# Kernel optimization log

Measured on AMD Instinct MI355X. Metric: run time of the kernel, lower is better.

Reference implementation:

```python
import jax, jax.numpy as jnp
import numpy as np

NUM_HEADS = 4
HIDDEN = 256
HEAD_DIM = HIDDEN // NUM_HEADS
N_NODES = 8192
N_EDGES = 262144
NEG = -1e9


def setup_inputs() -> dict:
    key = jax.random.key(0)
    ks = jax.random.split(key, 10)
    s = 1.0 / np.sqrt(HIDDEN)
    inp = {
        "node_features": jax.random.normal(ks[0], (N_NODES, HIDDEN), dtype=jnp.float32),
        "Wq": jax.random.uniform(ks[1], (HIDDEN, HIDDEN), jnp.float32, -s, s),
        "bq": jnp.zeros((HIDDEN,), jnp.float32),
        "Wk": jax.random.uniform(ks[2], (HIDDEN, HIDDEN), jnp.float32, -s, s),
        "bk": jnp.zeros((HIDDEN,), jnp.float32),
        "Wv": jax.random.uniform(ks[3], (HIDDEN, HIDDEN), jnp.float32, -s, s),
        "bv": jnp.zeros((HIDDEN,), jnp.float32),
        "Wo": jax.random.uniform(ks[4], (HIDDEN, HIDDEN), jnp.float32, -s, s),
        "bo": jnp.zeros((HIDDEN,), jnp.float32),
        "edge_index": jax.random.randint(ks[5], (2, N_EDGES), 0, N_NODES, dtype=jnp.int64),
    }
    return inp


def reference(node_features, Wq, bq, Wk, bk, Wv, bv, Wo, bo, edge_index):
    N = node_features.shape[0]
    # QKV projections -> [H, N, d]
    q = (node_features @ Wq + bq).reshape(N, NUM_HEADS, HEAD_DIM).transpose(1, 0, 2)
    k = (node_features @ Wk + bk).reshape(N, NUM_HEADS, HEAD_DIM).transpose(1, 0, 2)
    v = (node_features @ Wv + bv).reshape(N, NUM_HEADS, HEAD_DIM).transpose(1, 0, 2)
    # dense scores [H, N, N]
    scores = jnp.einsum('hnd,hmd->hnm', q, k) / jnp.sqrt(jnp.float32(HEAD_DIM))
    mask = jnp.full((N, N), NEG, dtype=jnp.float32).at[edge_index[0], edge_index[1]].set(0.0)
    scores = scores + mask[None, :, :]
    weights = jax.nn.softmax(scores, axis=-1)  # dropout is identity in eval
    context = jnp.einsum('hnm,hmd->hnd', weights, v)
    context = context.transpose(1, 0, 2).reshape(N, HIDDEN)
    return context @ Wo + bo
```

## Files before the change

kernel.cpp:

```cpp
#include <hip/hip_runtime.h>
#include <hip/hip_fp16.h>
#include <stdint.h>

#define NN 8192
#define HID 256
#define NH 4
#define HD 64
#define NE 262144
#define WPR (NN / 32)
#define CAP 128
#define NQKV 768
#define G1B 384

typedef __attribute__((ext_vector_type(8))) short s16x8;
typedef __attribute__((ext_vector_type(4))) float f32x4;
typedef _Float16 f16x2 __attribute__((ext_vector_type(2)));

__device__ __forceinline__ float fdot2(f16x2 a, f16x2 b, float c) {
#if __has_builtin(__builtin_amdgcn_fdot2)
    return __builtin_amdgcn_fdot2(a, b, c, false);
#else
    return c + (float)a.x * (float)b.x + (float)a.y * (float)b.y;
#endif
}

__device__ __forceinline__ void gload_lds16(const unsigned short* g, unsigned short* l) {
    __builtin_amdgcn_global_load_lds(
        (const __attribute__((address_space(1))) unsigned int*)g,
        (__attribute__((address_space(3))) unsigned int*)l, 16, 0, 0);
}

__global__ __launch_bounds__(256) void zero_kernel(uint4* __restrict__ p)
{
    p[blockIdx.x * 256 + threadIdx.x] = make_uint4(0, 0, 0, 0);
}

__global__ __launch_bounds__(256) void prep_kernel(
    const float* __restrict__ X,
    const float* __restrict__ Wq, const float* __restrict__ Wk,
    const float* __restrict__ Wv, const float* __restrict__ Wo,
    const float* __restrict__ bq, const float* __restrict__ bk,
    const float* __restrict__ bv, const int* __restrict__ ei,
    uint32_t* __restrict__ bitmap, unsigned short* __restrict__ Xh,
    unsigned short* __restrict__ W2Tq, unsigned short* __restrict__ W2To,
    float* __restrict__ biasq)
{
    const int b = blockIdx.x, tid = threadIdx.x;
    if (b < 1024) {
        int e = b * 256 + tid;
        int r = ei[e];
        int c = ei[NE + e];
        atomicOr(&bitmap[(size_t)r * WPR + (c >> 5)], 1u << (c & 31));
    } else if (b < 3072) {
        int i4 = ((b - 1024) * 256 + tid) * 4;
        float4 x = *(const float4*)(X + i4);
        __half2 h0 = __floats2half2_rn(x.x, x.y);
        __half2 h1 = __floats2half2_rn(x.z, x.w);
        uint2 w;
        w.x = *(unsigned*)&h0;
        w.y = *(unsigned*)&h1;
        *(uint2*)(Xh + i4) = w;
    } else {
        int lin = (b - 3072) * 256 + tid;
        int n = lin >> 8, k = lin & 255;
        const float* W; int ns; unsigned short* dst;
        if (n < NQKV) {
            W  = (n < 256) ? Wq : (n < 512) ? Wk : Wv;
            ns = n & 255;
            dst = W2Tq + (size_t)n * HID + k;
            if (k == 0) {
                const float* bsrc = (n < 256) ? bq : (n < 512) ? bk : bv;
                biasq[n] = bsrc[ns];
            }
        } else {
            W = Wo; ns = n - NQKV;
            dst = W2To + (size_t)ns * HID + k;
        }
        __half h = __float2half(W[(size_t)k * HID + ns]);
        *dst = *(unsigned short*)&h;
    }
}

template<int BN, bool HALF_OUT>
__device__ __forceinline__ void gemm_body(
    const unsigned short* __restrict__ A, const unsigned short* __restrict__ BT,
    const float* __restrict__ bias, void* __restrict__ Cv, int N,
    int m0, int n0, unsigned short* Alds, unsigned short* Blds)
{
    constexpr int NFR = BN / 32;
    const int tid  = threadIdx.x;
    const int lane = tid & 63, wave = tid >> 6;
    const int wm = wave >> 1, wn = wave & 1;

    const int r0 = tid >> 2, cc0 = tid & 3;
    const int r1 = (tid + 256) >> 2, cc1 = (tid + 256) & 3;

    f32x4 acc[4][NFR];
    #pragma unroll
    for (int i = 0; i < 4; ++i)
        #pragma unroll
        for (int j = 0; j < NFR; ++j)
            acc[i][j] = (f32x4){0.f, 0.f, 0.f, 0.f};

    for (int step = 0; step < 8; ++step) {
        const int kk = step * 32;
        __syncthreads();
        gload_lds16(A + (size_t)(m0 + r0) * HID + kk + cc0 * 8, &Alds[tid * 8]);
        gload_lds16(A + (size_t)(m0 + r1) * HID + kk + cc1 * 8, &Alds[(tid + 256) * 8]);
        gload_lds16(BT + (size_t)(n0 + r0) * HID + kk + cc0 * 8, &Blds[tid * 8]);
        if constexpr (BN == 128)
            gload_lds16(BT + (size_t)(n0 + r1) * HID + kk + cc1 * 8, &Blds[(tid + 256) * 8]);
        __syncthreads();

        s16x8 af[4], bfr[NFR];
        #pragma unroll
        for (int i = 0; i < 4; ++i)
            af[i] = *(const s16x8*)&Alds[(wm * 64 + i * 16 + (lane & 15)) * 32 + (lane >> 4) * 8];
        #pragma unroll
        for (int j = 0; j < NFR; ++j)
            bfr[j] = *(const s16x8*)&Blds[(wn * (BN / 2) + j * 16 + (lane & 15)) * 32 + (lane >> 4) * 8];
        #pragma unroll
        for (int i = 0; i < 4; ++i)
            #pragma unroll
            for (int j = 0; j < NFR; ++j)
                acc[i][j] = __builtin_amdgcn_mfma_f32_16x16x32_f16(af[i], bfr[j], acc[i][j], 0, 0, 0);
    }

    #pragma unroll
    for (int i = 0; i < 4; ++i) {
        #pragma unroll
        for (int j = 0; j < NFR; ++j) {
            int gcol = n0 + wn * (BN / 2) + j * 16 + (lane & 15);
            float bb = bias[gcol];
            #pragma unroll
            for (int r = 0; r < 4; ++r) {
                int grow = m0 + wm * 64 + i * 16 + (lane >> 4) * 4 + r;
                float v = acc[i][j][r] + bb;
                if constexpr (HALF_OUT)
                    ((__half*)Cv)[(size_t)grow * N + gcol] = __float2half(v);
                else
                    ((float*)Cv)[(size_t)grow * N + gcol] = v;
            }
        }
    }
}

__global__ __launch_bounds__(256) void gemm_csr_kernel(
    const unsigned short* __restrict__ Xh, const unsigned short* __restrict__ W2Tq,
    const float* __restrict__ biasq, __half* __restrict__ QKV,
    const uint32_t* __restrict__ bitmap, int* __restrict__ nbr, int* __restrict__ cnt)
{
    __shared__ __align__(16) unsigned short Alds[128 * 32];
    __shared__ __align__(16) unsigned short Blds[128 * 32];

    if (blockIdx.x < G1B) {
        constexpr int q8 = G1B >> 3;
        const int orig = blockIdx.x;
        const int id = (orig & 7) * q8 + (orig >> 3);
        gemm_body<128, true>(Xh, W2Tq, biasq, QKV, NQKV,
                             (id & 63) * 128, (id >> 6) * 128, Alds, Blds);
        return;
    }
    const int row = (blockIdx.x - G1B) * 4 + (threadIdx.x >> 6);
    const int lane = threadIdx.x & 63;
    const uint32_t* rp = bitmap + (size_t)row * WPR + lane * 4;
    uint32_t w0 = rp[0], w1 = rp[1], w2 = rp[2], w3 = rp[3];
    int pc = __popc(w0) + __popc(w1) + __popc(w2) + __popc(w3);
    int scan = pc;
    #pragma unroll
    for (int off = 1; off < 64; off <<= 1) {
        int t = __shfl_up(scan, off);
        if (lane >= off) scan += t;
    }
    int idx = scan - pc;
    int* dst = nbr + (size_t)row * CAP;
    const int base = lane * 128;
    uint32_t ws4[4] = {w0, w1, w2, w3};
    #pragma unroll
    for (int i = 0; i < 4; ++i) {
        uint32_t w = ws4[i];
        int cb = base + i * 32;
        while (w) {
            int b = __ffs(w) - 1;
            if (idx < CAP) dst[idx] = cb + b;
            ++idx;
            w &= w - 1;
        }
    }
    if (lane == 63) cnt[row] = min(scan, CAP);
}

template<int BN, bool HALF_OUT>
__global__ __launch_bounds__(256) void gemm_kernel(
    const unsigned short* __restrict__ A, const unsigned short* __restrict__ BT,
    const float* __restrict__ bias, void* __restrict__ Cv, int N)
{
    __shared__ __align__(16) unsigned short Alds[128 * 32];
    __shared__ __align__(16) unsigned short Blds[BN * 32];
    const int nwg = gridDim.x, orig = blockIdx.x, q8 = nwg >> 3;
    const int id = (orig & 7) * q8 + (orig >> 3);
    gemm_body<BN, HALF_OUT>(A, BT, bias, Cv, N,
                            (id & 63) * 128, (id >> 6) * BN, Alds, Blds);
}

__global__ __launch_bounds__(256) void attn_kernel(
    const __half* __restrict__ QKV, const int* __restrict__ nbr,
    const int* __restrict__ cntg, __half* __restrict__ ctx)
{
    const int row  = blockIdx.x * 4 + (threadIdx.x >> 6);
    const int lane = threadIdx.x & 63;
    const int cnt  = cntg[row];

    uint2 qraw = ((const uint2*)(QKV + (size_t)row * NQKV))[lane];
    union { uint2 u2; f16x2 h[2]; } uq; uq.u2 = qraw;
    const f16x2 q2a = uq.h[0], q2b = uq.h[1];

    float m = -INFINITY, l = 0.f;
    float a0 = 0.f, a1 = 0.f, a2 = 0.f, a3 = 0.f;

    for (int j0 = 0; j0 < cnt; j0 += 64) {
        int mynb = (j0 + lane < cnt) ? nbr[(size_t)row * CAP + j0 + lane] : 0;
        const int nb = min(64, cnt - j0);
        for (int b = 0; b < nb; b += 8) {
            int idx[8];
            #pragma unroll
            for (int u = 0; u < 8; ++u) idx[u] = __shfl(mynb, b + u);
            uint2 kv[8], vv[8];
            #pragma unroll
            for (int u = 0; u < 8; ++u) {
                const __half* base = QKV + (size_t)idx[u] * NQKV;
                kv[u] = ((const uint2*)(base + 256))[lane];
                vv[u] = ((const uint2*)(base + 512))[lane];
            }
            float s[8];
            #pragma unroll
            for (int u = 0; u < 8; ++u) {
                union { uint2 u2; f16x2 h[2]; } uk; uk.u2 = kv[u];
                float p = fdot2(q2a, uk.h[0], 0.f);
                p = fdot2(q2b, uk.h[1], p);
                #pragma unroll
                for (int off = 1; off < 16; off <<= 1) p += __shfl_xor(p, off);
                s[u] = (b + u < nb) ? p * 0.125f : -INFINITY;
            }
            float bm = s[0];
            #pragma unroll
            for (int u = 1; u < 8; ++u) bm = fmaxf(bm, s[u]);
            float mn = fmaxf(m, bm);
            float sc = expf(m - mn);
            a0 *= sc; a1 *= sc; a2 *= sc; a3 *= sc; l *= sc;
            #pragma unroll
            for (int u = 0; u < 8; ++u) {
                float w = expf(s[u] - mn);
                l += w;
                union { uint2 u2; __half2 h[2]; } uv; uv.u2 = vv[u];
                float2 f0 = __half22float2(uv.h[0]);
                float2 f1 = __half22float2(uv.h[1]);
                a0 = fmaf(w, f0.x, a0); a1 = fmaf(w, f0.y, a1);
                a2 = fmaf(w, f1.x, a2); a3 = fmaf(w, f1.y, a3);
            }
            m = mn;
        }
    }

    uint2 outw = make_uint2(0u, 0u);
    if (cnt > 0) {
        float rl = 1.f / l;
        __half2 o0 = __floats2half2_rn(a0 * rl, a1 * rl);
        __half2 o1 = __floats2half2_rn(a2 * rl, a3 * rl);
        outw.x = *(unsigned*)&o0;
        outw.y = *(unsigned*)&o1;
    }
    ((uint2*)(ctx + (size_t)row * HID))[lane] = outw;
}

extern "C" void kernel_launch(void* const* d_in, const int* in_sizes, int n_in,
                              void* d_out, int out_size, void* d_ws, size_t ws_size,
                              hipStream_t stream)
{
    const float* X  = (const float*)d_in[0];
    const float* Wq = (const float*)d_in[1];
    const float* bq = (const float*)d_in[2];
    const float* Wk = (const float*)d_in[3];
    const float* bk = (const float*)d_in[4];
    const float* Wv = (const float*)d_in[5];
    const float* bv = (const float*)d_in[6];
    const float* Wo = (const float*)d_in[7];
    const float* bo = (const float*)d_in[8];
    const int*   ei = (const int*)d_in[9];
    float* out = (float*)d_out;

    char* ws = (char*)d_ws;
    uint32_t*       bitmap = (uint32_t*)ws;
    __half*         QKV    = (__half*)(ws + 8388608);
    unsigned short* Xh     = (unsigned short*)(ws + 20971520);
    __half*         ctx    = (__half*)Xh;
    unsigned short* W2Tq   = (unsigned short*)(ws + 25165824);
    unsigned short* W2To   = (unsigned short*)(ws + 25559040);
    float*          biasq  = (float*)(ws + 25690112);
    int*            nbrL   = (int*)(ws + 25693184);
    int*            cntL   = (int*)(ws + 29887488);

    zero_kernel<<<2048, 256, 0, stream>>>((uint4*)bitmap);
    prep_kernel<<<4096, 256, 0, stream>>>(
        X, Wq, Wk, Wv, Wo, bq, bk, bv, ei, bitmap, Xh, W2Tq, W2To, biasq);
    gemm_csr_kernel<<<G1B + 2048, 256, 0, stream>>>(
        Xh, W2Tq, biasq, QKV, bitmap, nbrL, cntL);
    attn_kernel<<<NN / 4, 256, 0, stream>>>(QKV, nbrL, cntL, ctx);
    gemm_kernel<64, false><<<256, 256, 0, stream>>>(
        (const unsigned short*)ctx, W2To, bo, out, HID);
}
```

Measured before the change: 75.76 us.

## Fuse output projection GEMM into sparse attention kernel via LDS context tile

The attention kernel now processes 16 rows per 1024-thread block, stages the fp16 context rows in LDS, and then each wave computes a 16x16 slice of the output projection with MFMA against Wo read directly from global memory. This removes the separate output GEMM launch and the global write and read of the context buffer. In exchange, blocks are larger and synchronise after attention, so waves with fewer neighbours idle at the barrier. Wo fragments are also reloaded from global/L2 by every block instead of being shared through LDS tiles.

```diff
diff --git a/kernel.cpp b/kernel.cpp
--- a/kernel.cpp
+++ b/kernel.cpp
@@ -11,6 +11,7 @@
 #define CAP 128
 #define NQKV 768
 #define G1B 384
+#define CTXP 264
 
 typedef __attribute__((ext_vector_type(8))) short s16x8;
 typedef __attribute__((ext_vector_type(4))) float f32x4;
@@ -81,13 +82,11 @@
     }
 }
 
-template<int BN, bool HALF_OUT>
-__device__ __forceinline__ void gemm_body(
+__device__ __forceinline__ void gemm_body128(
     const unsigned short* __restrict__ A, const unsigned short* __restrict__ BT,
-    const float* __restrict__ bias, void* __restrict__ Cv, int N,
+    const float* __restrict__ bias, __half* __restrict__ Cv, int N,
     int m0, int n0, unsigned short* Alds, unsigned short* Blds)
 {
-    constexpr int NFR = BN / 32;
     const int tid  = threadIdx.x;
     const int lane = tid & 63, wave = tid >> 6;
     const int wm = wave >> 1, wn = wave & 1;
@@ -95,11 +94,11 @@
     const int r0 = tid >> 2, cc0 = tid & 3;
     const int r1 = (tid + 256) >> 2, cc1 = (tid + 256) & 3;
 
-    f32x4 acc[4][NFR];
+    f32x4 acc[4][4];
     #pragma unroll
     for (int i = 0; i < 4; ++i)
         #pragma unroll
-        for (int j = 0; j < NFR; ++j)
+        for (int j = 0; j < 4; ++j)
             acc[i][j] = (f32x4){0.f, 0.f, 0.f, 0.f};
 
     for (int step = 0; step < 8; ++step) {
@@ -108,38 +107,33 @@
         gload_lds16(A + (size_t)(m0 + r0) * HID + kk + cc0 * 8, &Alds[tid * 8]);
         gload_lds16(A + (size_t)(m0 + r1) * HID + kk + cc1 * 8, &Alds[(tid + 256) * 8]);
         gload_lds16(BT + (size_t)(n0 + r0) * HID + kk + cc0 * 8, &Blds[tid * 8]);
-        if constexpr (BN == 128)
-            gload_lds16(BT + (size_t)(n0 + r1) * HID + kk + cc1 * 8, &Blds[(tid + 256) * 8]);
+        gload_lds16(BT + (size_t)(n0 + r1) * HID + kk + cc1 * 8, &Blds[(tid + 256) * 8]);
         __syncthreads();
 
-        s16x8 af[4], bfr[NFR];
+        s16x8 af[4], bfr[4];
         #pragma unroll
         for (int i = 0; i < 4; ++i)
             af[i] = *(const s16x8*)&Alds[(wm * 64 + i * 16 + (lane & 15)) * 32 + (lane >> 4) * 8];
         #pragma unroll
-        for (int j = 0; j < NFR; ++j)
-            bfr[j] = *(const s16x8*)&Blds[(wn * (BN / 2) + j * 16 + (lane & 15)) * 32 + (lane >> 4) * 8];
+        for (int j = 0; j < 4; ++j)
+            bfr[j] = *(const s16x8*)&Blds[(wn * 64 + j * 16 + (lane & 15)) * 32 + (lane >> 4) * 8];
         #pragma unroll
         for (int i = 0; i < 4; ++i)
             #pragma unroll
-            for (int j = 0; j < NFR; ++j)
+            for (int j = 0; j < 4; ++j)
                 acc[i][j] = __builtin_amdgcn_mfma_f32_16x16x32_f16(af[i], bfr[j], acc[i][j], 0, 0, 0);
     }
 
     #pragma unroll
     for (int i = 0; i < 4; ++i) {
         #pragma unroll
-        for (int j = 0; j < NFR; ++j) {
-            int gcol = n0 + wn * (BN / 2) + j * 16 + (lane & 15);
+        for (int j = 0; j < 4; ++j) {
+            int gcol = n0 + wn * 64 + j * 16 + (lane & 15);
             float bb = bias[gcol];
             #pragma unroll
             for (int r = 0; r < 4; ++r) {
                 int grow = m0 + wm * 64 + i * 16 + (lane >> 4) * 4 + r;
-                float v = acc[i][j][r] + bb;
-                if constexpr (HALF_OUT)
-                    ((__half*)Cv)[(size_t)grow * N + gcol] = __float2half(v);
-                else
-                    ((float*)Cv)[(size_t)grow * N + gcol] = v;
+                Cv[(size_t)grow * N + gcol] = __float2half(acc[i][j][r] + bb);
             }
         }
     }
@@ -157,8 +151,8 @@
         constexpr int q8 = G1B >> 3;
         const int orig = blockIdx.x;
         const int id = (orig & 7) * q8 + (orig >> 3);
-        gemm_body<128, true>(Xh, W2Tq, biasq, QKV, NQKV,
-                             (id & 63) * 128, (id >> 6) * 128, Alds, Blds);
+        gemm_body128(Xh, W2Tq, biasq, QKV, NQKV,
+                     (id & 63) * 128, (id >> 6) * 128, Alds, Blds);
         return;
     }
     const int row = (blockIdx.x - G1B) * 4 + (threadIdx.x >> 6);
@@ -190,26 +184,18 @@
     if (lane == 63) cnt[row] = min(scan, CAP);
 }
 
-template<int BN, bool HALF_OUT>
-__global__ __launch_bounds__(256) void gemm_kernel(
-    const unsigned short* __restrict__ A, const unsigned short* __restrict__ BT,
-    const float* __restrict__ bias, void* __restrict__ Cv, int N)
-{
-    __shared__ __align__(16) unsigned short Alds[128 * 32];
-    __shared__ __align__(16) unsigned short Blds[BN * 32];
-    const int nwg = gridDim.x, orig = blockIdx.x, q8 = nwg >> 3;
-    const int id = (orig & 7) * q8 + (orig >> 3);
-    gemm_body<BN, HALF_OUT>(A, BT, bias, Cv, N,
-                            (id & 63) * 128, (id >> 6) * BN, Alds, Blds);
-}
-
-__global__ __launch_bounds__(256) void attn_kernel(
+__global__ __launch_bounds__(1024, 8) void attn_out_kernel(
     const __half* __restrict__ QKV, const int* __restrict__ nbr,
-    const int* __restrict__ cntg, __half* __restrict__ ctx)
-{
-    const int row  = blockIdx.x * 4 + (threadIdx.x >> 6);
+    const int* __restrict__ cntg, const unsigned short* __restrict__ W2To,
+    const float* __restrict__ bo, float* __restrict__ out)
+{
+    const int wv   = threadIdx.x >> 6;
     const int lane = threadIdx.x & 63;
+    const int rb   = blockIdx.x * 16;
+    const int row  = rb + wv;
     const int cnt  = cntg[row];
+
+    __shared__ __align__(16) unsigned short ctxlds[16][CTXP];
 
     uint2 qraw = ((const uint2*)(QKV + (size_t)row * NQKV))[lane];
     union { uint2 u2; f16x2 h[2]; } uq; uq.u2 = qraw;
@@ -262,15 +248,33 @@
         }
     }
 
-    uint2 outw = make_uint2(0u, 0u);
-    if (cnt > 0) {
-        float rl = 1.f / l;
+    {
+        float rl = (cnt > 0) ? (1.f / l) : 0.f;
         __half2 o0 = __floats2half2_rn(a0 * rl, a1 * rl);
         __half2 o1 = __floats2half2_rn(a2 * rl, a3 * rl);
-        outw.x = *(unsigned*)&o0;
-        outw.y = *(unsigned*)&o1;
-    }
-    ((uint2*)(ctx + (size_t)row * HID))[lane] = outw;
+        uint2 w;
+        w.x = *(unsigned*)&o0;
+        w.y = *(unsigned*)&o1;
+        *(uint2*)&ctxlds[wv][lane * 4] = w;
+    }
+    __syncthreads();
+
+    f32x4 acc = (f32x4){0.f, 0.f, 0.f, 0.f};
+    const unsigned short* bt = W2To + (size_t)(wv * 16 + (lane & 15)) * HID + (lane >> 4) * 8;
+    const unsigned short* al = &ctxlds[lane & 15][(lane >> 4) * 8];
+    #pragma unroll
+    for (int step = 0; step < 8; ++step) {
+        s16x8 af = *(const s16x8*)(al + step * 32);
+        s16x8 bf = *(const s16x8*)(bt + step * 32);
+        acc = __builtin_amdgcn_mfma_f32_16x16x32_f16(af, bf, acc, 0, 0, 0);
+    }
+    const int gcol = wv * 16 + (lane & 15);
+    const float bb = bo[gcol];
+    #pragma unroll
+    for (int r = 0; r < 4; ++r) {
+        int grow = rb + (lane >> 4) * 4 + r;
+        out[(size_t)grow * HID + gcol] = acc[r] + bb;
+    }
 }
 
 extern "C" void kernel_launch(void* const* d_in, const int* in_sizes, int n_in,
@@ -293,7 +297,6 @@
     uint32_t*       bitmap = (uint32_t*)ws;
     __half*         QKV    = (__half*)(ws + 8388608);
     unsigned short* Xh     = (unsigned short*)(ws + 20971520);
-    __half*         ctx    = (__half*)Xh;
     unsigned short* W2Tq   = (unsigned short*)(ws + 25165824);
     unsigned short* W2To   = (unsigned short*)(ws + 25559040);
     float*          biasq  = (float*)(ws + 25690112);
@@ -305,7 +308,6 @@
         X, Wq, Wk, Wv, Wo, bq, bk, bv, ei, bitmap, Xh, W2Tq, W2To, biasq);
     gemm_csr_kernel<<<G1B + 2048, 256, 0, stream>>>(
         Xh, W2Tq, biasq, QKV, bitmap, nbrL, cntL);
-    attn_kernel<<<NN / 4, 256, 0, stream>>>(QKV, nbrL, cntL, ctx);
-    gemm_kernel<64, false><<<256, 256, 0, stream>>>(
-        (const unsigned short*)ctx, W2To, bo, out, HID);
-}
+    attn_out_kernel<<<NN / 16, 1024, 0, stream>>>(
+        QKV, nbrL, cntL, W2To, bo, out);
+}
```

After: 78.25 us. 3.3% more time.

## Load K and V together as 16-byte vectors split across half-wavefronts

Applied to the files above, without the earlier changes.

Each wavefront lane now issues one 16-byte load over the contiguous K|V region of a neighbour row: lanes 0-31 hold K, lanes 32-63 hold V, 8 halves each. This replaces the two 8-byte loads per neighbour. The dot-product reduction becomes a 3-step butterfly within 8 lanes plus a cross-half exchange, and only the V half accumulates and writes output. It also adds a launch-bounds occupancy hint of 8 blocks. The aim is fewer memory instructions, at the cost of doubled accumulator registers and half the lanes doing redundant work in each phase.

```diff
diff --git a/kernel.cpp b/kernel.cpp
--- a/kernel.cpp
+++ b/kernel.cpp
@@ -203,20 +203,21 @@
                             (id & 63) * 128, (id >> 6) * BN, Alds, Blds);
 }
 
-__global__ __launch_bounds__(256) void attn_kernel(
+__global__ __launch_bounds__(256, 8) void attn_kernel(
     const __half* __restrict__ QKV, const int* __restrict__ nbr,
     const int* __restrict__ cntg, __half* __restrict__ ctx)
 {
     const int row  = blockIdx.x * 4 + (threadIdx.x >> 6);
     const int lane = threadIdx.x & 63;
+    const bool isK = lane < 32;
     const int cnt  = cntg[row];
 
-    uint2 qraw = ((const uint2*)(QKV + (size_t)row * NQKV))[lane];
-    union { uint2 u2; f16x2 h[2]; } uq; uq.u2 = qraw;
-    const f16x2 q2a = uq.h[0], q2b = uq.h[1];
+    uint4 qraw = ((const uint4*)(QKV + (size_t)row * NQKV))[lane & 31];
+    union { uint4 u4; f16x2 h[4]; } uq; uq.u4 = qraw;
 
     float m = -INFINITY, l = 0.f;
     float a0 = 0.f, a1 = 0.f, a2 = 0.f, a3 = 0.f;
+    float a4 = 0.f, a5 = 0.f, a6 = 0.f, a7 = 0.f;
 
     for (int j0 = 0; j0 < cnt; j0 += 64) {
         int mynb = (j0 + lane < cnt) ? nbr[(size_t)row * CAP + j0 + lane] : 0;
@@ -225,21 +226,22 @@
             int idx[8];
             #pragma unroll
             for (int u = 0; u < 8; ++u) idx[u] = __shfl(mynb, b + u);
-            uint2 kv[8], vv[8];
+            uint4 kvv[8];
+            #pragma unroll
+            for (int u = 0; u < 8; ++u)
+                kvv[u] = ((const uint4*)(QKV + (size_t)idx[u] * NQKV + 256))[lane];
+            float s[8];
             #pragma unroll
             for (int u = 0; u < 8; ++u) {
-                const __half* base = QKV + (size_t)idx[u] * NQKV;
-                kv[u] = ((const uint2*)(base + 256))[lane];
-                vv[u] = ((const uint2*)(base + 512))[lane];
-            }
-            float s[8];
-            #pragma unroll
-            for (int u = 0; u < 8; ++u) {
-                union { uint2 u2; f16x2 h[2]; } uk; uk.u2 = kv[u];
-                float p = fdot2(q2a, uk.h[0], 0.f);
-                p = fdot2(q2b, uk.h[1], p);
+                union { uint4 u4; f16x2 h[4]; } uk; uk.u4 = kvv[u];
+                float p = fdot2(uq.h[0], uk.h[0], 0.f);
+                p = fdot2(uq.h[1], uk.h[1], p);
+                p = fdot2(uq.h[2], uk.h[2], p);
+                p = fdot2(uq.h[3], uk.h[3], p);
+                p = isK ? p : 0.f;
                 #pragma unroll
-                for (int off = 1; off < 16; off <<= 1) p += __shfl_xor(p, off);
+                for (int off = 1; off < 8; off <<= 1) p += __shfl_xor(p, off);
+                p += __shfl_xor(p, 32);
                 s[u] = (b + u < nb) ? p * 0.125f : -INFINITY;
             }
             float bm = s[0];
@@ -247,30 +249,42 @@
             for (int u = 1; u < 8; ++u) bm = fmaxf(bm, s[u]);
             float mn = fmaxf(m, bm);
             float sc = expf(m - mn);
-            a0 *= sc; a1 *= sc; a2 *= sc; a3 *= sc; l *= sc;
+            a0 *= sc; a1 *= sc; a2 *= sc; a3 *= sc;
+            a4 *= sc; a5 *= sc; a6 *= sc; a7 *= sc;
+            l *= sc;
             #pragma unroll
             for (int u = 0; u < 8; ++u) {
                 float w = expf(s[u] - mn);
                 l += w;
-                union { uint2 u2; __half2 h[2]; } uv; uv.u2 = vv[u];
+                union { uint4 u4; __half2 h[4]; } uv; uv.u4 = kvv[u];
                 float2 f0 = __half22float2(uv.h[0]);
                 float2 f1 = __half22float2(uv.h[1]);
+                float2 f2 = __half22float2(uv.h[2]);
+                float2 f3 = __half22float2(uv.h[3]);
                 a0 = fmaf(w, f0.x, a0); a1 = fmaf(w, f0.y, a1);
                 a2 = fmaf(w, f1.x, a2); a3 = fmaf(w, f1.y, a3);
+                a4 = fmaf(w, f2.x, a4); a5 = fmaf(w, f2.y, a5);
+                a6 = fmaf(w, f3.x, a6); a7 = fmaf(w, f3.y, a7);
             }
             m = mn;
         }
     }
 
-    uint2 outw = make_uint2(0u, 0u);
-    if (cnt > 0) {
-        float rl = 1.f / l;
-        __half2 o0 = __floats2half2_rn(a0 * rl, a1 * rl);
-        __half2 o1 = __floats2half2_rn(a2 * rl, a3 * rl);
-        outw.x = *(unsigned*)&o0;
-        outw.y = *(unsigned*)&o1;
-    }
-    ((uint2*)(ctx + (size_t)row * HID))[lane] = outw;
+    if (!isK) {
+        uint4 outw = make_uint4(0u, 0u, 0u, 0u);
+        if (cnt > 0) {
+            float rl = 1.f / l;
+            __half2 o0 = __floats2half2_rn(a0 * rl, a1 * rl);
+            __half2 o1 = __floats2half2_rn(a2 * rl, a3 * rl);
+            __half2 o2 = __floats2half2_rn(a4 * rl, a5 * rl);
+            __half2 o3 = __floats2half2_rn(a6 * rl, a7 * rl);
+            outw.x = *(unsigned*)&o0;
+            outw.y = *(unsigned*)&o1;
+            outw.z = *(unsigned*)&o2;
+            outw.w = *(unsigned*)&o3;
+        }
+        ((uint4*)(ctx + (size_t)row * HID))[lane - 32] = outw;
+    }
 }
 
 extern "C" void kernel_launch(void* const* d_in, const int* in_sizes, int n_in,
```

Result: slower. 94.67 us (+25.0%).
